# Kernel tuning notes

Hardware: AMD Instinct MI355X
Metric: run time of the kernel (lower is better)

The kernel has to match this reference:

```python
import jax, jax.numpy as jnp
import numpy as np

K = 3
STRIDE = 1
PAD = K // 2
GN_GROUPS = 32
EPS = 1e-5


def _conv(x, w, b, stride, pad):
    y = jax.lax.conv_general_dilated(
        x, w, window_strides=(stride, stride),
        padding=[(pad, pad), (pad, pad)],
        dimension_numbers=("NCHW", "OIHW", "NCHW"))
    return y + b[None, :, None, None]


def _bilinear_gather(img, ys, xs):
    # img: [B,C,H,W]; ys/xs: [B,P,Ho,Wo] float sampling coords (zero padding outside)
    B, C, H, W = img.shape
    y0 = jnp.floor(ys)
    x0 = jnp.floor(xs)
    y1, x1 = y0 + 1.0, x0 + 1.0
    wy1 = ys - y0  # weight toward y1
    wx1 = xs - x0
    wy0 = 1.0 - wy1
    wx0 = 1.0 - wx1
    img_flat = img.reshape(B, C, H * W)

    def corner(yc, xc, wgt):
        yi = yc.astype(jnp.int32)
        xi = xc.astype(jnp.int32)
        valid = (yi >= 0) & (yi < H) & (xi >= 0) & (xi < W)
        idx = jnp.clip(yi, 0, H - 1) * W + jnp.clip(xi, 0, W - 1)  # [B,P,Ho,Wo]
        Bp, P, Ho, Wo = idx.shape
        idx_f = jnp.broadcast_to(idx.reshape(B, 1, P * Ho * Wo), (B, C, P * Ho * Wo))
        vals = jnp.take_along_axis(img_flat, idx_f, axis=2).reshape(B, C, P, Ho, Wo)
        w_eff = jnp.where(valid, wgt, 0.0)[:, None]  # [B,1,P,Ho,Wo]
        return vals * w_eff

    out = (corner(y0, x0, wy0 * wx0) + corner(y0, x1, wy0 * wx1)
           + corner(y1, x0, wy1 * wx0) + corner(y1, x1, wy1 * wx1))
    return out  # [B,C,P,Ho,Wo]


def _deform_conv_gn_relu(x, w_off, b_off, w, b, gamma, beta):
    B, C_in, H, W = x.shape
    C_out = w.shape[0]
    P = K * K
    # offset-predicting conv: [B, 2*P, Ho, Wo], channel order (dy0,dx0,dy1,dx1,...)
    off = _conv(x, w_off, b_off, STRIDE, PAD)
    Ho, Wo = off.shape[2], off.shape[3]
    off = off.reshape(B, P, 2, Ho, Wo)
    dy, dx = off[:, :, 0], off[:, :, 1]  # [B,P,Ho,Wo]
    ky, kx = jnp.meshgrid(jnp.arange(K, dtype=x.dtype), jnp.arange(K, dtype=x.dtype), indexing="ij")
    ky, kx = ky.reshape(P), kx.reshape(P)
    base_y = (jnp.arange(Ho, dtype=x.dtype) * STRIDE - PAD)
    base_x = (jnp.arange(Wo, dtype=x.dtype) * STRIDE - PAD)
    ys = base_y[None, None, :, None] + ky[None, :, None, None] + dy
    xs = base_x[None, None, None, :] + kx[None, :, None, None] + dx
    cols = _bilinear_gather(x, ys, xs)  # [B,C_in,P,Ho,Wo]
    y = jnp.einsum("bcphw,ocp->bohw", cols, w.reshape(C_out, C_in, P)) + b[None, :, None, None]
    # GroupNorm(32, C_out)
    G = GN_GROUPS
    yg = y.reshape(B, G, (C_out // G) * Ho * Wo)
    mu = yg.mean(axis=2, keepdims=True)
    var = yg.var(axis=2, keepdims=True)
    yn = ((yg - mu) * jax.lax.rsqrt(var + EPS)).reshape(B, C_out, Ho, Wo)
    yn = yn * gamma[None, :, None, None] + beta[None, :, None, None]
    return jax.nn.relu(yn)


def setup_inputs() -> dict:
    key = jax.random.key(0)
    ks = jax.random.split(key, 7)
    B, C_in, C_out, H, W = 4, 256, 256, 64, 64
    P = K * K
    fan = C_in * P
    x = jax.random.normal(ks[0], (B, C_in, H, W), dtype=jnp.float32)
    w_off = jax.random.normal(ks[1], (2 * P, C_in, K, K), dtype=jnp.float32) * 0.01
    b_off = jnp.zeros((2 * P,), dtype=jnp.float32)
    w = jax.random.normal(ks[2], (C_out, C_in, K, K), dtype=jnp.float32) / np.sqrt(fan)
    b = jax.random.normal(ks[3], (C_out,), dtype=jnp.float32) * 0.01
    gamma = jnp.ones((C_out,), dtype=jnp.float32)
    beta = jnp.zeros((C_out,), dtype=jnp.float32)
    return {"x": x, "w_off": w_off, "b_off": b_off, "w": w, "b": b, "gamma": gamma, "beta": beta}


def reference(x, w_off, b_off, w, b, gamma, beta):
    return _deform_conv_gn_relu(x, w_off, b_off, w, b, gamma, beta)
```

## Files before the change

### kernel.cpp

```cpp
#include <hip/hip_runtime.h>
#include <hip/hip_bf16.h>

using bf16 = __hip_bfloat16;
typedef __attribute__((ext_vector_type(4))) float f32x4;
typedef __attribute__((ext_vector_type(2))) float f32x2;
typedef __attribute__((ext_vector_type(8))) __bf16 bf16x8;
typedef __attribute__((ext_vector_type(4))) __bf16 bf16x4;

#define CIN 256
#define COUT 256
#define HW 4096
#define NB 4
#define NTOT 16384
#define KDIM 2304

__global__ __launch_bounds__(256) void k_transpose(const float* __restrict__ x,
                                                   float* __restrict__ xt) {
  __shared__ float t[32][33];
  int bid = blockIdx.x;
  int ct = bid & 7;
  int hwt = (bid >> 3) & 127;
  int b = bid >> 10;
  int tx = threadIdx.x & 31, ty = threadIdx.x >> 5;
  int c0 = ct * 32, hw0 = hwt * 32;
  const float* xb = x + (size_t)b * CIN * HW;
#pragma unroll
  for (int i = 0; i < 32; i += 8)
    t[ty + i][tx] = xb[(size_t)(c0 + ty + i) * HW + hw0 + tx];
  __syncthreads();
  float* xo = xt + ((size_t)b * HW + hw0) * CIN + c0;
#pragma unroll
  for (int i = 0; i < 32; i += 8)
    xo[(size_t)(ty + i) * CIN + tx] = t[tx][ty + i];
}

__global__ __launch_bounds__(256) void k_prepwt(const float* __restrict__ wof,
                                                float* __restrict__ wt) {
  int i = blockIdx.x * 256 + threadIdx.x;
  if (i >= 18 * CIN * 9) return;
  int oc = i % 18;
  int cp = i / 18;
  int c = cp / 9, p = cp % 9;
  wt[i] = wof[((size_t)oc * CIN + c) * 9 + p];
}

__global__ __launch_bounds__(256) void k_convoff2(const float* __restrict__ x,
                                                  const float* __restrict__ wt,
                                                  float* __restrict__ part) {
  __shared__ float lds[8][6][68];
  int bid = blockIdx.x;
  int chunk = bid & 7;
  int rt = (bid >> 3) & 15;
  int b = bid >> 7;
  int tid = threadIdx.x;
  int wq = tid & 63, r = tid >> 6;
  int h0 = rt * 4;
  int c0 = chunk * 32;

  if (tid < 96) {
    int cl = tid / 12, rem = tid % 12;
    lds[cl][rem >> 1][(rem & 1) ? 66 : 1] = 0.f;
  }

  float acc[18];
#pragma unroll
  for (int o = 0; o < 18; ++o) acc[o] = 0.f;

  int ch = tid >> 5, l32 = tid & 31;
  const float* xb = x + (size_t)b * CIN * HW;

  for (int cs = 0; cs < 32; cs += 8) {
    __syncthreads();
    const float* xp = xb + (size_t)(c0 + cs + ch) * HW;
#pragma unroll
    for (int r6 = 0; r6 < 6; ++r6) {
      int hh = h0 - 1 + r6;
      f32x2 v = {0.f, 0.f};
      if ((unsigned)hh < 64u) v = *(const f32x2*)(xp + hh * 64 + l32 * 2);
      *(f32x2*)&lds[ch][r6][2 + l32 * 2] = v;
    }
    __syncthreads();
#pragma unroll
    for (int cl = 0; cl < 8; ++cl) {
      int c = c0 + cs + cl;
      const float* wc = wt + (size_t)c * 9 * 18;
      float xv[9];
#pragma unroll
      for (int ky = 0; ky < 3; ++ky)
#pragma unroll
        for (int kx = 0; kx < 3; ++kx)
          xv[ky * 3 + kx] = lds[cl][r + ky][1 + wq + kx];
#pragma unroll
      for (int p = 0; p < 9; ++p)
#pragma unroll
        for (int o = 0; o < 18; ++o)
          acc[o] = fmaf(xv[p], wc[p * 18 + o], acc[o]);
    }
  }

  float* pp = part + (size_t)chunk * (NB * 18 * HW) + (size_t)b * 18 * HW +
              (h0 + r) * 64 + wq;
#pragma unroll
  for (int o = 0; o < 18; ++o) pp[(size_t)o * HW] = acc[o];
}

__global__ __launch_bounds__(256) void k_offreduce(const float* __restrict__ part,
                                                   const float* __restrict__ boff,
                                                   float* __restrict__ off) {
  int i = blockIdx.x * 256 + threadIdx.x;
  int e0 = i * 4;
  int oc = (e0 >> 12) % 18;
  float bo = boff[oc];
  f32x4 s = {bo, bo, bo, bo};
#pragma unroll
  for (int c = 0; c < 8; ++c) s += *(const f32x4*)(part + (size_t)c * (NB * 18 * HW) + e0);
  *(f32x4*)(off + e0) = s;
}

__global__ __launch_bounds__(256) void k_prepw(const float* __restrict__ w,
                                               bf16* __restrict__ A) {
  int i = blockIdx.x * 256 + threadIdx.x;
  int o = i / KDIM, r = i % KDIM;
  int p = r >> 8, c = r & 255;
  A[i] = __float2bfloat16(w[((size_t)o * 256 + c) * 9 + p]);
}

__global__ __launch_bounds__(256) void k_gather(const float* __restrict__ xt,
                                                const float* __restrict__ off,
                                                bf16* __restrict__ colsT) {
  int tid = threadIdx.x;
  int wv = tid >> 6, l = tid & 63;
  int n = blockIdx.x * 4 + wv;
  int hw = n & 4095;
  int b = n >> 12;
  int h = hw >> 6, wq = hw & 63;
  const float* xtb = xt + (size_t)b * HW * CIN + l * 4;
  const float* offb = off + (size_t)b * 18 * HW + hw;
  bf16* outp = colsT + (size_t)n * KDIM + l * 4;
#pragma unroll
  for (int p = 0; p < 9; ++p) {
    float dy = offb[(size_t)(2 * p) * HW];
    float dx = offb[(size_t)(2 * p + 1) * HW];
    float ysf = (float)(h - 1 + p / 3) + dy;
    float xsf = (float)(wq - 1 + p % 3) + dx;
    float y0f = floorf(ysf), x0f = floorf(xsf);
    float wy1 = ysf - y0f, wx1 = xsf - x0f;
    float wy0 = 1.f - wy1, wx0 = 1.f - wx1;
    int y0 = (int)y0f, x0 = (int)x0f;
    int y1 = y0 + 1, x1 = x0 + 1;
    float w00 = wy0 * wx0, w01 = wy0 * wx1, w10 = wy1 * wx0, w11 = wy1 * wx1;
    bool vy0 = (unsigned)y0 < 64u, vy1 = (unsigned)y1 < 64u;
    bool vx0 = (unsigned)x0 < 64u, vx1 = (unsigned)x1 < 64u;
    w00 = (vy0 && vx0) ? w00 : 0.f;
    w01 = (vy0 && vx1) ? w01 : 0.f;
    w10 = (vy1 && vx0) ? w10 : 0.f;
    w11 = (vy1 && vx1) ? w11 : 0.f;
    int y0c = min(max(y0, 0), 63), y1c = min(max(y1, 0), 63);
    int x0c = min(max(x0, 0), 63), x1c = min(max(x1, 0), 63);
    f32x4 v00 = *(const f32x4*)(xtb + (size_t)(y0c * 64 + x0c) * CIN);
    f32x4 v01 = *(const f32x4*)(xtb + (size_t)(y0c * 64 + x1c) * CIN);
    f32x4 v10 = *(const f32x4*)(xtb + (size_t)(y1c * 64 + x0c) * CIN);
    f32x4 v11 = *(const f32x4*)(xtb + (size_t)(y1c * 64 + x1c) * CIN);
    f32x4 v;
#pragma unroll
    for (int k = 0; k < 4; ++k)
      v[k] = w00 * v00[k] + w01 * v01[k] + w10 * v10[k] + w11 * v11[k];
    bf16x4 o;
#pragma unroll
    for (int k = 0; k < 4; ++k) o[k] = (__bf16)v[k];
    *(bf16x4*)(outp + p * 256) = o;
  }
}

__global__ __launch_bounds__(256) void k_gemm(const bf16* __restrict__ A,
                                              const bf16* __restrict__ Bt,
                                              const float* __restrict__ bias,
                                              float* __restrict__ Y) {
  __shared__ bf16 As[2][128 * 64];
  __shared__ bf16 Bs[2][64 * 64];
  int bid = blockIdx.x;
  int swz = (bid & 7) * 64 + (bid >> 3);
  int mt = swz & 1, nt = swz >> 1;
  int m0 = mt * 128, n0 = nt * 64;
  int tid = threadIdx.x;
  int lane = tid & 63;
  int wave = tid >> 6;
  int wr = (wave >> 1) * 64, wc = (wave & 1) * 32;
  f32x4 acc[4][2];
#pragma unroll
  for (int i = 0; i < 4; ++i)
#pragma unroll
    for (int j = 0; j < 2; ++j) acc[i][j] = (f32x4){0.f, 0.f, 0.f, 0.f};

  int srow = tid >> 3;
  int skdst = (tid & 7) * 8;
  int sksrc = ((tid & 7) ^ ((tid >> 3) & 7)) * 8;
  auto stage = [&](int buf, int k0) {
#pragma unroll
    for (int ps = 0; ps < 4; ++ps) {
      int r = srow + ps * 32;
      __builtin_amdgcn_global_load_lds(
          (const __attribute__((address_space(1))) void*)(A + (size_t)(m0 + r) * KDIM + k0 + sksrc),
          (__attribute__((address_space(3))) void*)(&As[buf][r * 64 + skdst]), 16, 0, 0);
    }
#pragma unroll
    for (int ps = 0; ps < 2; ++ps) {
      int r = srow + ps * 32;
      __builtin_amdgcn_global_load_lds(
          (const __attribute__((address_space(1))) void*)(Bt + (size_t)(n0 + r) * KDIM + k0 + sksrc),
          (__attribute__((address_space(3))) void*)(&Bs[buf][r * 64 + skdst]), 16, 0, 0);
    }
  };

  stage(0, 0);
  int rl = lane & 15;
  int kb = (lane >> 4) * 8;
  int xorv = (rl & 7) * 8;
  for (int kt = 0; kt < KDIM / 64; ++kt) {
    __syncthreads();
    if (kt + 1 < KDIM / 64) stage((kt + 1) & 1, (kt + 1) * 64);
    const bf16* as = As[kt & 1];
    const bf16* bs = Bs[kt & 1];
#pragma unroll
    for (int kh = 0; kh < 2; ++kh) {
      int kc = (kh * 32 + kb) ^ xorv;
      bf16x8 af[4], bfr[2];
#pragma unroll
      for (int i = 0; i < 4; ++i)
        af[i] = *(const bf16x8*)(as + (wr + i * 16 + rl) * 64 + kc);
#pragma unroll
      for (int j = 0; j < 2; ++j)
        bfr[j] = *(const bf16x8*)(bs + (wc + j * 16 + rl) * 64 + kc);
#pragma unroll
      for (int i = 0; i < 4; ++i)
#pragma unroll
        for (int j = 0; j < 2; ++j)
          acc[i][j] = __builtin_amdgcn_mfma_f32_16x16x32_bf16(af[i], bfr[j], acc[i][j], 0, 0, 0);
    }
  }
  int cl = lane & 15, rg = (lane >> 4) * 4;
#pragma unroll
  for (int i = 0; i < 4; ++i) {
    int ob = m0 + wr + i * 16 + rg;
#pragma unroll
    for (int j = 0; j < 2; ++j) {
      int nn = n0 + wc + j * 16 + cl;
#pragma unroll
      for (int r = 0; r < 4; ++r) {
        Y[(size_t)(ob + r) * NTOT + nn] = acc[i][j][r] + bias[ob + r];
      }
    }
  }
}

__global__ __launch_bounds__(256) void k_gnstats(const float* __restrict__ Y,
                                                 const float* __restrict__ gamma,
                                                 const float* __restrict__ beta,
                                                 float* __restrict__ sc,
                                                 float* __restrict__ sh) {
  int b = blockIdx.x >> 5, g = blockIdx.x & 31;
  int tid = threadIdx.x;
  float s = 0.f, s2 = 0.f;
  for (int i = tid; i < 8192; i += 256) {
    int ol = i >> 10, pos = i & 1023;
    f32x4 v = *(const f32x4*)(Y + (size_t)(g * 8 + ol) * NTOT + b * HW + pos * 4);
#pragma unroll
    for (int k = 0; k < 4; ++k) {
      s += v[k];
      s2 = fmaf(v[k], v[k], s2);
    }
  }
#pragma unroll
  for (int o = 32; o > 0; o >>= 1) {
    s += __shfl_down(s, o);
    s2 += __shfl_down(s2, o);
  }
  __shared__ float red[8];
  int wv = tid >> 6;
  if ((tid & 63) == 0) { red[wv] = s; red[wv + 4] = s2; }
  __syncthreads();
  if (tid == 0) {
    float S = red[0] + red[1] + red[2] + red[3];
    float S2 = red[4] + red[5] + red[6] + red[7];
    float mu = S * (1.f / 32768.f);
    float var = S2 * (1.f / 32768.f) - mu * mu;
    red[0] = mu;
    red[1] = rsqrtf(var + 1e-5f);
  }
  __syncthreads();
  if (tid < 8) {
    int o = g * 8 + tid;
    float mu = red[0], rs = red[1];
    float gm = gamma[o];
    sc[b * 256 + o] = rs * gm;
    sh[b * 256 + o] = beta[o] - mu * rs * gm;
  }
}

__global__ __launch_bounds__(256) void k_apply(const float* __restrict__ Y,
                                               const float* __restrict__ sc,
                                               const float* __restrict__ sh,
                                               float* __restrict__ out) {
  int i = blockIdx.x * 256 + threadIdx.x;
  int hw4 = i & 1023;
  int o = (i >> 10) & 255;
  int b = i >> 18;
  f32x4 v = *(const f32x4*)(Y + (size_t)o * NTOT + b * HW + hw4 * 4);
  float s = sc[b * 256 + o], t = sh[b * 256 + o];
  f32x4 r;
#pragma unroll
  for (int k = 0; k < 4; ++k) r[k] = fmaxf(v[k] * s + t, 0.f);
  *(f32x4*)(out + (size_t)i * 4) = r;
}

extern "C" void kernel_launch(void* const* d_in, const int* in_sizes, int n_in,
                              void* d_out, int out_size, void* d_ws, size_t ws_size,
                              hipStream_t stream) {
  const float* x = (const float*)d_in[0];
  const float* w_off = (const float*)d_in[1];
  const float* b_off = (const float*)d_in[2];
  const float* w = (const float*)d_in[3];
  const float* bias = (const float*)d_in[4];
  const float* gamma = (const float*)d_in[5];
  const float* beta = (const float*)d_in[6];
  float* out = (float*)d_out;
  char* ws = (char*)d_ws;

  float* xt = (float*)(ws);
  float* offb = (float*)(ws + 16777216);
  bf16* Abf = (bf16*)(ws + 16777216 + 1179648);
  bf16* colsT = (bf16*)(ws + 16777216 + 2 * 1179648);
  float* Y = (float*)(ws + 16777216 + 2 * 1179648 + 75497472);
  float* sc = (float*)(ws + 2 * 16777216 + 2 * 1179648 + 75497472);
  float* sh = sc + 1024;

  float* wt = (float*)colsT;
  float* part = (float*)((char*)colsT + 262144);

  k_transpose<<<4096, 256, 0, stream>>>(x, xt);
  k_prepwt<<<162, 256, 0, stream>>>(w_off, wt);
  k_convoff2<<<512, 256, 0, stream>>>(x, wt, part);
  k_offreduce<<<288, 256, 0, stream>>>(part, b_off, offb);
  k_prepw<<<2304, 256, 0, stream>>>(w, Abf);
  k_gather<<<4096, 256, 0, stream>>>(xt, offb, colsT);
  k_gemm<<<512, 256, 0, stream>>>(Abf, colsT, bias, Y);
  k_gnstats<<<128, 256, 0, stream>>>(Y, gamma, beta, sc, sh);
  k_apply<<<4096, 256, 0, stream>>>(Y, sc, sh, out);
}
```

Measured before the change: 142.9 us.

## Fuse GroupNorm statistics into GEMM epilogue and enlarge GEMM N-tile to 128

The GEMM epilogue now accumulates per-group sum and sum of squares with wave shuffles and atomics, which removes the separate k_gnstats pass that re-read Y. The apply kernel computes the scale and shift from those sums itself. The GEMM tile also grows from 128x64 to 128x128, so the grid halves to 256 blocks. That raises data reuse per block but leaves fewer blocks than the 256 CUs can use well, and it adds a memset plus atomic contention.

Result: slower. 157.1 us (+10.0%).

```diff
diff --git a/kernel.cpp b/kernel.cpp
--- a/kernel.cpp
+++ b/kernel.cpp
@@ -175,22 +175,24 @@
 __global__ __launch_bounds__(256) void k_gemm(const bf16* __restrict__ A,
                                               const bf16* __restrict__ Bt,
                                               const float* __restrict__ bias,
-                                              float* __restrict__ Y) {
+                                              float* __restrict__ Y,
+                                              float* __restrict__ gsum,
+                                              float* __restrict__ gsq) {
   __shared__ bf16 As[2][128 * 64];
-  __shared__ bf16 Bs[2][64 * 64];
+  __shared__ bf16 Bs[2][128 * 64];
   int bid = blockIdx.x;
-  int swz = (bid & 7) * 64 + (bid >> 3);
+  int swz = (bid & 7) * 32 + (bid >> 3);
   int mt = swz & 1, nt = swz >> 1;
-  int m0 = mt * 128, n0 = nt * 64;
+  int m0 = mt * 128, n0 = nt * 128;
   int tid = threadIdx.x;
   int lane = tid & 63;
   int wave = tid >> 6;
-  int wr = (wave >> 1) * 64, wc = (wave & 1) * 32;
-  f32x4 acc[4][2];
+  int wr = (wave >> 1) * 64, wc = (wave & 1) * 64;
+  f32x4 acc[4][4];
 #pragma unroll
   for (int i = 0; i < 4; ++i)
 #pragma unroll
-    for (int j = 0; j < 2; ++j) acc[i][j] = (f32x4){0.f, 0.f, 0.f, 0.f};
+    for (int j = 0; j < 4; ++j) acc[i][j] = (f32x4){0.f, 0.f, 0.f, 0.f};
 
   int srow = tid >> 3;
   int skdst = (tid & 7) * 8;
@@ -204,7 +206,7 @@
           (__attribute__((address_space(3))) void*)(&As[buf][r * 64 + skdst]), 16, 0, 0);
     }
 #pragma unroll
-    for (int ps = 0; ps < 2; ++ps) {
+    for (int ps = 0; ps < 4; ++ps) {
       int r = srow + ps * 32;
       __builtin_amdgcn_global_load_lds(
           (const __attribute__((address_space(1))) void*)(Bt + (size_t)(n0 + r) * KDIM + k0 + sksrc),
@@ -224,89 +226,68 @@
 #pragma unroll
     for (int kh = 0; kh < 2; ++kh) {
       int kc = (kh * 32 + kb) ^ xorv;
-      bf16x8 af[4], bfr[2];
+      bf16x8 af[4], bfr[4];
 #pragma unroll
       for (int i = 0; i < 4; ++i)
         af[i] = *(const bf16x8*)(as + (wr + i * 16 + rl) * 64 + kc);
 #pragma unroll
-      for (int j = 0; j < 2; ++j)
+      for (int j = 0; j < 4; ++j)
         bfr[j] = *(const bf16x8*)(bs + (wc + j * 16 + rl) * 64 + kc);
 #pragma unroll
       for (int i = 0; i < 4; ++i)
 #pragma unroll
-        for (int j = 0; j < 2; ++j)
+        for (int j = 0; j < 4; ++j)
           acc[i][j] = __builtin_amdgcn_mfma_f32_16x16x32_bf16(af[i], bfr[j], acc[i][j], 0, 0, 0);
     }
   }
   int cl = lane & 15, rg = (lane >> 4) * 4;
+  int b = n0 >> 12;
 #pragma unroll
   for (int i = 0; i < 4; ++i) {
-    int ob = m0 + wr + i * 16 + rg;
-#pragma unroll
-    for (int j = 0; j < 2; ++j) {
+    int obase = m0 + wr + i * 16;
+    int ob = obase + rg;
+    float s = 0.f, s2 = 0.f;
+#pragma unroll
+    for (int j = 0; j < 4; ++j) {
       int nn = n0 + wc + j * 16 + cl;
 #pragma unroll
       for (int r = 0; r < 4; ++r) {
-        Y[(size_t)(ob + r) * NTOT + nn] = acc[i][j][r] + bias[ob + r];
+        float yv = acc[i][j][r] + bias[ob + r];
+        Y[(size_t)(ob + r) * NTOT + nn] = yv;
+        s += yv;
+        s2 = fmaf(yv, yv, s2);
       }
     }
-  }
-}
-
-__global__ __launch_bounds__(256) void k_gnstats(const float* __restrict__ Y,
-                                                 const float* __restrict__ gamma,
-                                                 const float* __restrict__ beta,
-                                                 float* __restrict__ sc,
-                                                 float* __restrict__ sh) {
-  int b = blockIdx.x >> 5, g = blockIdx.x & 31;
-  int tid = threadIdx.x;
-  float s = 0.f, s2 = 0.f;
-  for (int i = tid; i < 8192; i += 256) {
-    int ol = i >> 10, pos = i & 1023;
-    f32x4 v = *(const f32x4*)(Y + (size_t)(g * 8 + ol) * NTOT + b * HW + pos * 4);
-#pragma unroll
-    for (int k = 0; k < 4; ++k) {
-      s += v[k];
-      s2 = fmaf(v[k], v[k], s2);
-    }
-  }
-#pragma unroll
-  for (int o = 32; o > 0; o >>= 1) {
-    s += __shfl_down(s, o);
-    s2 += __shfl_down(s2, o);
-  }
-  __shared__ float red[8];
-  int wv = tid >> 6;
-  if ((tid & 63) == 0) { red[wv] = s; red[wv + 4] = s2; }
-  __syncthreads();
-  if (tid == 0) {
-    float S = red[0] + red[1] + red[2] + red[3];
-    float S2 = red[4] + red[5] + red[6] + red[7];
-    float mu = S * (1.f / 32768.f);
-    float var = S2 * (1.f / 32768.f) - mu * mu;
-    red[0] = mu;
-    red[1] = rsqrtf(var + 1e-5f);
-  }
-  __syncthreads();
-  if (tid < 8) {
-    int o = g * 8 + tid;
-    float mu = red[0], rs = red[1];
-    float gm = gamma[o];
-    sc[b * 256 + o] = rs * gm;
-    sh[b * 256 + o] = beta[o] - mu * rs * gm;
+#pragma unroll
+    for (int mk = 1; mk <= 16; mk <<= 1) {
+      s += __shfl_xor(s, mk);
+      s2 += __shfl_xor(s2, mk);
+    }
+    if ((lane & 31) == 0) {
+      int g = (obase >> 3) + (lane >> 5);
+      atomicAdd(&gsum[b * 32 + g], s);
+      atomicAdd(&gsq[b * 32 + g], s2);
+    }
   }
 }
 
 __global__ __launch_bounds__(256) void k_apply(const float* __restrict__ Y,
-                                               const float* __restrict__ sc,
-                                               const float* __restrict__ sh,
+                                               const float* __restrict__ gsum,
+                                               const float* __restrict__ gsq,
+                                               const float* __restrict__ gamma,
+                                               const float* __restrict__ beta,
                                                float* __restrict__ out) {
   int i = blockIdx.x * 256 + threadIdx.x;
   int hw4 = i & 1023;
   int o = (i >> 10) & 255;
   int b = i >> 18;
+  int g = o >> 3;
+  float mu = gsum[b * 32 + g] * (1.f / 32768.f);
+  float var = gsq[b * 32 + g] * (1.f / 32768.f) - mu * mu;
+  float rs = rsqrtf(var + 1e-5f);
+  float s = rs * gamma[o];
+  float t = beta[o] - mu * s;
   f32x4 v = *(const f32x4*)(Y + (size_t)o * NTOT + b * HW + hw4 * 4);
-  float s = sc[b * 256 + o], t = sh[b * 256 + o];
   f32x4 r;
 #pragma unroll
   for (int k = 0; k < 4; ++k) r[k] = fmaxf(v[k] * s + t, 0.f);
@@ -331,19 +312,19 @@
   bf16* Abf = (bf16*)(ws + 16777216 + 1179648);
   bf16* colsT = (bf16*)(ws + 16777216 + 2 * 1179648);
   float* Y = (float*)(ws + 16777216 + 2 * 1179648 + 75497472);
-  float* sc = (float*)(ws + 2 * 16777216 + 2 * 1179648 + 75497472);
-  float* sh = sc + 1024;
+  float* gsum = (float*)(ws + 2 * 16777216 + 2 * 1179648 + 75497472);
+  float* gsq = gsum + 128;
 
   float* wt = (float*)colsT;
   float* part = (float*)((char*)colsT + 262144);
 
+  hipMemsetAsync(gsum, 0, 2 * 128 * sizeof(float), stream);
   k_transpose<<<4096, 256, 0, stream>>>(x, xt);
   k_prepwt<<<162, 256, 0, stream>>>(w_off, wt);
   k_convoff2<<<512, 256, 0, stream>>>(x, wt, part);
   k_offreduce<<<288, 256, 0, stream>>>(part, b_off, offb);
   k_prepw<<<2304, 256, 0, stream>>>(w, Abf);
   k_gather<<<4096, 256, 0, stream>>>(xt, offb, colsT);
-  k_gemm<<<512, 256, 0, stream>>>(Abf, colsT, bias, Y);
-  k_gnstats<<<128, 256, 0, stream>>>(Y, gamma, beta, sc, sh);
-  k_apply<<<4096, 256, 0, stream>>>(Y, sc, sh, out);
-}
+  k_gemm<<<256, 256, 0, stream>>>(Abf, colsT, bias, Y, gsum, gsq);
+  k_apply<<<4096, 256, 0, stream>>>(Y, gsum, gsq, gamma, beta, out);
+}
```
